# Optimization experiments

Hardware: AMD Instinct MI355X
Metric: run time of the kernel (lower is better)

## Reference

```python
import jax, jax.numpy as jnp
import numpy as np

PI = 3.1415927410125732
N = 4096
L = 1.28e-3          # box side [m]
VEL = 5e-7
RC = 3.15e-6         # Rc = diameter/2
RR = 8e-6
RO = 2.5e-5
RA = np.inf
DT_TRANS = 1.4e-14   # DT (translational diffusion)
DR = 0.0028
GAMMA = 25.0
DT = 0.2             # timestep dt
COLL_ITERS = 30      # fixed cap for collision-resolution do-while (orig caps at 1000)


def setup_inputs() -> dict:
    key = jax.random.key(0)
    ks = jax.random.split(key, 7)
    pos_re = jax.random.uniform(ks[0], (N,), jnp.float32) * L
    pos_im = jax.random.uniform(ks[1], (N,), jnp.float32) * L
    ang = jax.random.uniform(ks[2], (N,), jnp.float32, -PI, PI)
    ori_re = jnp.cos(ang)
    ori_im = jnp.sin(ang)
    deltas = jax.random.uniform(ks[3], (N,), jnp.float32) * 0.5
    rot_noise = jax.random.normal(ks[4], (N,), jnp.float32)
    tn_re = jax.random.normal(ks[5], (N,), jnp.float32)
    tn_im = jax.random.normal(ks[6], (N,), jnp.float32)
    return {"pos_re": pos_re, "pos_im": pos_im, "ori_re": ori_re, "ori_im": ori_im,
            "deltas": deltas, "rot_noise": rot_noise, "tn_re": tn_re, "tn_im": tn_im}


def _wrap(diff):
    # torch get_anglediff wrap: (-2pi,2pi) -> ~(-pi,pi)
    diff = jnp.where(diff <= -PI, jnp.mod(diff, PI), diff)
    return diff - (diff >= PI).astype(diff.dtype) * (2.0 * PI)


def _anglediff(a, b):
    return _wrap(jnp.angle(a) - jnp.angle(b))


def _cossim(a, b):
    # nn.CosineSimilarity(dim=1, eps=1e-14) on view_as_real vectors
    dot = a.real * b.real + a.imag * b.imag
    na = jnp.maximum(jnp.abs(a), 1e-14)
    nb = jnp.maximum(jnp.abs(b), 1e-14)
    return dot / (na * nb)


def _mvc(W, z):
    # real [n,n] mask @ complex [n] vector
    return W @ z.real + 1j * (W @ z.imag)


def _solve_collisions(pos):
    n = pos.shape[0]
    eye_f = jnp.eye(n, dtype=jnp.float32)
    eye_c = eye_f.astype(pos.dtype)

    def step(p):
        diff = p[None, :] - p[:, None] + eye_c  # [i,j] = pos_j - pos_i; diag dummy 1 (nan-safe)
        absd = jnp.abs(diff)
        coll = absd <= (2.0 * RC - eye_f)       # diag threshold negative -> self excluded
        move = jnp.where(coll, diff / jnp.where(coll, absd, 1.0) * ((2.1 * RC - absd) * 0.5), 0.0)
        return p - move.sum(axis=1), coll.sum()

    def body(carry, _):
        p, cont = carry
        p_new, ncoll = step(p)
        p = jnp.where(cont, p_new, p)           # do-while: apply move, then continue if collisions
        return (p, jnp.logical_and(cont, ncoll > 0)), None

    body = jax.checkpoint(body)
    (pos, _), _ = jax.lax.scan(body, (pos, jnp.array(True)), None, length=COLL_ITERS)
    return pos


def _forward(pos_re, pos_im, ori_re, ori_im, deltas, rot_noise, tn_re, tn_im):
    pos = (pos_re + 1j * pos_im).astype(jnp.complex64)
    ori = (ori_re + 1j * ori_im).astype(jnp.complex64)
    n = pos.shape[0]
    eye_b = jnp.eye(n, dtype=bool)

    # pairwise |pos_i - pos_j|; diag made 1 to keep abs() grad-safe (diag is masked out / re-added below)
    dists = jnp.abs(pos[:, None] - pos[None, :] + jnp.eye(n, dtype=pos.dtype))
    mask_rr = (dists <= RR) & ~eye_b              # repulsion zone, self excluded (eye subtracted in orig)
    mask_ro = (dists <= RO + RC) | eye_b          # orientation zone, self included (diag dist 0 in orig)
    mask_ra = (dists <= RA + RC) | eye_b          # Ra = inf -> all ones

    # alpha == 2*pi exactly -> within_view branch skipped (matches original)
    ang = jnp.angle(ori)
    abs_ad = jnp.abs(_wrap(ang[:, None] - ang[None, :]))
    in_front = abs_ad < PI / 2

    Wrr = (mask_rr & in_front).astype(jnp.float32)
    Wro = mask_ro.astype(jnp.float32)
    Wra = mask_ra.astype(jnp.float32)

    n_r = Wrr.sum(axis=1)
    S = _mvc(Wrr, pos) / jnp.maximum(n_r, 1.0) - pos * jnp.sign(n_r)
    d = -S

    n_a = Wra.sum(axis=1)
    cms = _mvc(Wra, pos) / jnp.maximum(n_a, 1.0)
    Ps = cms - pos * jnp.sign(n_a)

    osum = _mvc(Wro, ori)
    left = Ps * jnp.exp(1j * deltas)
    right = Ps * jnp.exp(-1j * deltas)

    # T (=300) >= T_release (=200): choose best turn by cosine similarity
    best = jnp.where(_cossim(left, osum) >= _cossim(right, osum), left, right)

    has_rep = jnp.abs(d) > 0.0
    d_safe = jnp.where(has_rep, d, jnp.ones_like(d))
    att = jnp.where(has_rep, _anglediff(d_safe, ori), _anglediff(best, ori))

    s2dr = np.float32(np.sqrt(2.0 * DR))
    sdt = np.float32(np.sqrt(DT))
    rot = jnp.exp(1j * (DT * GAMMA * DR * jnp.sin(att) + rot_noise * s2dr * sdt))

    # complex standard normal: real/imag each N(0, 1/sqrt(2))
    tnoise = (tn_re + 1j * tn_im) * np.float32(np.sqrt(0.5)) * np.float32(np.sqrt(2.0 * DT_TRANS))
    trans = DT * VEL * ori + tnoise * sdt

    new_pos = _solve_collisions(pos + trans)
    new_ori = ori * rot

    c2r = lambda z: jnp.stack([z.real, z.imag], axis=-1)
    # [5, N, 2]: positions, orientations, orientation_sums, leftturns, rightturns (real views)
    return jnp.stack([c2r(new_pos), c2r(new_ori), c2r(osum), c2r(left), c2r(right)], axis=0)


def reference(pos_re, pos_im, ori_re, ori_im, deltas, rot_noise, tn_re, tn_im):
    return _forward(pos_re, pos_im, ori_re, ori_im, deltas, rot_noise, tn_re, tn_im)
```

## Files before the change

### kernel.cpp

```cpp
#include <hip/hip_runtime.h>

#define NPART 4096
#define PI_F 3.1415927410125732f
#define TWO_PI_F 6.2831854820251465f
#define SENT 4096
#define TILE_F 1.6e-4f
#define HALO_F 2.15e-4f
#define CAP 1280
#define LSENT CAP

__device__ __forceinline__ float wrapf(float d) {
    if (d <= -PI_F) {
        d = fmodf(d, PI_F);
        if (d < 0.0f) d += PI_F;
    }
    if (d >= PI_F) d -= TWO_PI_F;
    return d;
}

__global__ __launch_bounds__(512)
void k_interact(const float* __restrict__ pr, const float* __restrict__ pim,
                const float* __restrict__ orr, const float* __restrict__ oim,
                const float* __restrict__ deltas,
                const float* __restrict__ rot_noise,
                const float* __restrict__ tn_re, const float* __restrict__ tn_im,
                float* __restrict__ out,
                uint2* __restrict__ recQuad, int* __restrict__ recC,
                unsigned short* __restrict__ recNbr16) {
    constexpr float RR_F  = 8e-6f;
    constexpr float RR2   = RR_F * RR_F;
    constexpr float ROC_F = (float)(2.5e-5 + 3.15e-6);
    constexpr float ROC2  = ROC_F * ROC_F;
    constexpr float CUT_F = 14.3e-6f;
    constexpr float CUT2  = CUT_F * CUT_F;

    __shared__ float2 lsP[NPART];
    __shared__ float2 lsO[NPART];
    __shared__ float part[12][64];
    __shared__ float red[12][8];
    __shared__ int ncnt[16];
    __shared__ unsigned short nbrL[16 * 16];

    int tid = threadIdx.x;
    int li = tid & 7, sl = tid >> 3;
    int i0 = blockIdx.x * 16 + li;
    int i1 = i0 + 8;

    if (tid < 16) ncnt[tid] = 0;

    float pxA = pr[i0], pyA = pim[i0], oxA = orr[i0], oyA = oim[i0];
    float pxB = pr[i1], pyB = pim[i1], oxB = orr[i1], oyB = oim[i1];

    float nAr = 0.0f, SAre = 0.0f, SAim = 0.0f, oAre = 0.0f, oAim = 0.0f;
    float nBr = 0.0f, SBre = 0.0f, SBim = 0.0f, oBre = 0.0f, oBim = 0.0f;
    float cs_re = 0.0f, cs_im = 0.0f;

#pragma unroll
    for (int k = 0; k < 8; ++k) {
        int j = k * 512 + tid;
        float jr = pr[j], ji = pim[j];
        lsP[j] = make_float2(jr, ji);
        lsO[j] = make_float2(orr[j], oim[j]);
        cs_re += jr; cs_im += ji;
    }
    __syncthreads();

    for (int c = 0; c < 8; ++c) {
#pragma unroll
        for (int t = 0; t < 8; ++t) {
            int jj = c * 512 + sl * 8 + ((t + sl) & 7);
            int j = jj;
            float2 pv = lsP[jj];
            float drA = pxA - pv.x, diA = pyA - pv.y;
            float d2A = drA * drA + diA * diA;
            float drB = pxB - pv.x, diB = pyB - pv.y;
            float d2B = drB * drB + diB * diB;
            if (__any((d2A <= ROC2) | (d2B <= ROC2))) {
                float2 ov = lsO[jj];
                if (d2A <= ROC2) { oAre += ov.x; oAim += ov.y; }
                float dotA = oxA * ov.x + oyA * ov.y;
                if ((d2A <= RR2) & (dotA > 0.0f) & (j != i0)) {
                    nAr += 1.0f; SAre += pv.x; SAim += pv.y;
                }
                if (d2A <= CUT2 && j != i0) {
                    int slot = atomicAdd(&ncnt[li], 1);
                    if (slot < 16) nbrL[li * 16 + slot] = (unsigned short)j;
                }
                if (d2B <= ROC2) { oBre += ov.x; oBim += ov.y; }
                float dotB = oxB * ov.x + oyB * ov.y;
                if ((d2B <= RR2) & (dotB > 0.0f) & (j != i1)) {
                    nBr += 1.0f; SBre += pv.x; SBim += pv.y;
                }
                if (d2B <= CUT2 && j != i1) {
                    int slot = atomicAdd(&ncnt[li + 8], 1);
                    if (slot < 16) nbrL[(li + 8) * 16 + slot] = (unsigned short)j;
                }
            }
        }
    }

    {
        float v0 = nAr, v1 = SAre, v2 = SAim, v3 = oAre, v4 = oAim;
        float v5 = nBr, v6 = SBre, v7 = SBim, v8 = oBre, v9 = oBim;
        float v10 = cs_re, v11 = cs_im;
#define RED3(v) { v += __shfl_xor(v, 8); v += __shfl_xor(v, 16); v += __shfl_xor(v, 32); }
        RED3(v0) RED3(v1) RED3(v2) RED3(v3) RED3(v4) RED3(v5)
        RED3(v6) RED3(v7) RED3(v8) RED3(v9) RED3(v10) RED3(v11)
#undef RED3
        int lane = tid & 63, wv = tid >> 6;
        if (lane < 8) {
            int col = wv * 8 + lane;
            part[0][col] = v0;  part[1][col] = v1;  part[2][col] = v2;
            part[3][col] = v3;  part[4][col] = v4;  part[5][col] = v5;
            part[6][col] = v6;  part[7][col] = v7;  part[8][col] = v8;
            part[9][col] = v9;  part[10][col] = v10; part[11][col] = v11;
        }
    }
    __syncthreads();
    if (tid < 8) {
#pragma unroll
        for (int av = 0; av < 12; ++av) {
            float s = 0.0f;
#pragma unroll
            for (int w = 0; w < 8; ++w) s += part[av][w * 8 + tid];
            red[av][tid] = s;
        }
    }
    __syncthreads();

    if (tid < 16) {
        int i = blockIdx.x * 16 + tid;
        float n_r, S_re, S_im, o_re, o_im, px, py, ox, oy;
        if (tid < 8) {
            n_r = red[0][tid]; S_re = red[1][tid]; S_im = red[2][tid];
            o_re = red[3][tid]; o_im = red[4][tid];
            px = pxA; py = pyA; ox = oxA; oy = oyA;
        } else {
            int g = tid - 8;
            n_r = red[5][g]; S_re = red[6][g]; S_im = red[7][g];
            o_re = red[8][g]; o_im = red[9][g];
            px = pxB; py = pyB; ox = oxB; oy = oyB;
        }

        float csr_ = 0.0f, csi_ = 0.0f;
#pragma unroll
        for (int k = 0; k < 8; ++k) { csr_ += red[10][k]; csi_ += red[11][k]; }

        float maxnr = fmaxf(n_r, 1.0f);
        float sgn = (n_r > 0.0f) ? 1.0f : 0.0f;
        float Sre = S_re / maxnr - px * sgn;
        float Sim = S_im / maxnr - py * sgn;
        float d_re = -Sre, d_im = -Sim;

        float cmsx = csr_ * (1.0f / 4096.0f);
        float cmsy = csi_ * (1.0f / 4096.0f);
        float Ps_re = cmsx - px;
        float Ps_im = cmsy - py;

        float dl = deltas[i];
        float cd = cosf(dl), sd = sinf(dl);
        float l_re = Ps_re * cd - Ps_im * sd;
        float l_im = Ps_re * sd + Ps_im * cd;
        float r_re = Ps_re * cd + Ps_im * sd;
        float r_im = Ps_im * cd - Ps_re * sd;

        float nb   = fmaxf(hypotf(o_re, o_im), 1e-14f);
        float na_l = fmaxf(hypotf(l_re, l_im), 1e-14f);
        float na_r = fmaxf(hypotf(r_re, r_im), 1e-14f);
        float csl = (l_re * o_re + l_im * o_im) / (na_l * nb);
        float csr2 = (r_re * o_re + r_im * o_im) / (na_r * nb);
        float b_re = (csl >= csr2) ? l_re : r_re;
        float b_im = (csl >= csr2) ? l_im : r_im;

        float ai = atan2f(oy, ox);
        bool has_rep = (d_re != 0.0f) || (d_im != 0.0f);
        float att;
        if (has_rep) att = wrapf(atan2f(d_im, d_re) - ai);
        else         att = wrapf(atan2f(b_im, b_re) - ai);

        constexpr float GDD  = (float)(0.2 * 25.0 * 0.0028);
        constexpr float S2DR = 0.07483314773547883f;
        constexpr float SDT  = 0.44721359549995793f;
        float theta = GDD * sinf(att) + (rot_noise[i] * S2DR) * SDT;
        float rr_ = cosf(theta), ri_ = sinf(theta);

        float no_re = ox * rr_ - oy * ri_;
        float no_im = ox * ri_ + oy * rr_;

        constexpr float DTVEL = (float)(0.2 * 5e-7);
        constexpr float C1 = 0.70710678118654752f;
        constexpr float C2 = 1.6733200530681511e-07f;
        float t_re = DTVEL * ox + ((tn_re[i] * C1) * C2) * SDT;
        float t_im = DTVEL * oy + ((tn_im[i] * C1) * C2) * SDT;
        float p0x = px + t_re, p0y = py + t_im;

        float2* o2 = (float2*)out;
        o2[i]            = make_float2(p0x, p0y);
        o2[1 * 4096 + i] = make_float2(no_re, no_im);
        o2[2 * 4096 + i] = make_float2(o_re, o_im);
        o2[3 * 4096 + i] = make_float2(l_re, l_im);
        o2[4 * 4096 + i] = make_float2(r_re, r_im);

        int c = min(ncnt[tid], 16);
        unsigned q0 = (c > 0) ? nbrL[tid * 16 + 0] : (unsigned)SENT;
        unsigned q1 = (c > 1) ? nbrL[tid * 16 + 1] : (unsigned)SENT;
        unsigned q2 = (c > 2) ? nbrL[tid * 16 + 2] : (unsigned)SENT;
        unsigned q3 = (c > 3) ? nbrL[tid * 16 + 3] : (unsigned)SENT;
        recQuad[i] = make_uint2(q0 | (q1 << 16), q2 | (q3 << 16));
        recC[i] = c;
        if (c > 4) {
            int cp = (c + 3) & ~3;
            for (int m = 4; m < cp; ++m)
                recNbr16[i * 16 + m] = (m < c) ? nbrL[tid * 16 + m]
                                               : (unsigned short)SENT;
        }
    }
}

__global__ __launch_bounds__(256)
void k_coll_tiled(const uint2* __restrict__ recQuad, const int* __restrict__ recC,
                  const unsigned short* __restrict__ recNbr16,
                  float* __restrict__ out) {
    constexpr float TWO_RC  = (float)(2.0 * 3.15e-6);
    constexpr float TWO_RC2 = TWO_RC * TWO_RC;
    constexpr float C21RC   = (float)(2.1 * 3.15e-6);

    __shared__ float2 lpos[CAP + 1];
    __shared__ unsigned short g2l[NPART];
    __shared__ unsigned short lgid[CAP];
    __shared__ uint2 lquad[CAP];
    __shared__ unsigned char lc[CAP];
    __shared__ unsigned char lown[CAP];
    __shared__ short lpool[CAP];
    __shared__ unsigned short pool[96 * 16];
    __shared__ int cnt, poolCnt, flg[2];

    int tid = threadIdx.x;
    int tx = blockIdx.x & 7, ty = blockIdx.x >> 3;
    float x0 = tx * TILE_F, y0 = ty * TILE_F;
    float xlo = (tx == 0) ? -1e9f : x0 - HALO_F;
    float xhi = (tx == 7) ?  1e9f : x0 + TILE_F + HALO_F;
    float ylo = (ty == 0) ? -1e9f : y0 - HALO_F;
    float yhi = (ty == 7) ?  1e9f : y0 + TILE_F + HALO_F;

    if (tid == 0) {
        cnt = 0; poolCnt = 0; flg[0] = 0; flg[1] = 0;
        lpos[LSENT] = make_float2(1e9f, 1e9f);
    }
    __syncthreads();

    const float2* o2in = (const float2*)out;
    for (int g = tid; g < NPART; g += 256) {
        float2 p = o2in[g];
        unsigned short l = 0xFFFF;
        if (p.x >= xlo && p.x < xhi && p.y >= ylo && p.y < yhi) {
            int s = atomicAdd(&cnt, 1);
            if (s < CAP) {
                l = (unsigned short)s;
                lpos[s] = p;
                lgid[s] = (unsigned short)g;
                int ox = min(7, max(0, (int)floorf(p.x * (1.0f / TILE_F))));
                int oy = min(7, max(0, (int)floorf(p.y * (1.0f / TILE_F))));
                lown[s] = (ox == tx && oy == ty) ? 1 : 0;
            }
        }
        g2l[g] = l;
    }
    __syncthreads();
    int n = min(cnt, CAP);

    for (int l = tid; l < n; l += 256) {
        int g = lgid[l];
        uint2 q = recQuad[g];
        int c = recC[g];
        unsigned short a[4] = { (unsigned short)(q.x & 0xffff), (unsigned short)(q.x >> 16),
                                (unsigned short)(q.y & 0xffff), (unsigned short)(q.y >> 16) };
        unsigned short b[4];
#pragma unroll
        for (int k = 0; k < 4; ++k) {
            unsigned short t = (a[k] >= NPART) ? (unsigned short)0xFFFF : g2l[a[k]];
            b[k] = (t == 0xFFFF) ? (unsigned short)LSENT : t;
        }
        lquad[l] = make_uint2((unsigned)b[0] | ((unsigned)b[1] << 16),
                              (unsigned)b[2] | ((unsigned)b[3] << 16));
        lc[l] = (unsigned char)c;
        short prow = -1;
        if (c > 4) {
            int r = atomicAdd(&poolCnt, 1);
            if (r < 96) {
                prow = (short)r;
                int cp = (c + 3) & ~3;
                for (int m = 4; m < cp; ++m) {
                    unsigned short aa = recNbr16[g * 16 + m];
                    unsigned short t = (aa >= NPART) ? (unsigned short)0xFFFF : g2l[aa];
                    pool[r * 16 + m] = (t == 0xFFFF) ? (unsigned short)LSENT : t;
                }
            }
        }
        lpool[l] = prow;
    }
    __syncthreads();

    float nx[5], ny[5];
    int ncs[5];
    for (int it = 0; it < 12; ++it) {
#pragma unroll
        for (int s = 0; s < 5; ++s) {
            ncs[s] = 0;
            int l = s * 256 + tid;
            if (l < n) {
                int c = lc[l];
                if (c > 0) {
                    float2 me = lpos[l];
                    float px = me.x, py = me.y;
                    float mre = 0.0f, mim = 0.0f;
                    int nc = 0;
                    uint2 q = lquad[l];
                    float2 q0 = lpos[q.x & 0xffff], q1 = lpos[q.x >> 16];
                    float2 q2 = lpos[q.y & 0xffff], q3 = lpos[q.y >> 16];
#define COLL_ONE(qq)                                                    \
                    {                                                   \
                        float dr = (qq).x - px, di = (qq).y - py;       \
                        float d2 = dr * dr + di * di;                   \
                        if (d2 <= TWO_RC2) {                            \
                            float a = sqrtf(d2);                        \
                            float mm = (C21RC - a) * 0.5f / a;          \
                            mre += dr * mm; mim += di * mm; ++nc;       \
                        }                                               \
                    }
                    COLL_ONE(q0) COLL_ONE(q1) COLL_ONE(q2) COLL_ONE(q3)
                    for (int m0 = 4; m0 < c; m0 += 4) {
                        int j0, j1, j2, j3;
                        if (lpool[l] >= 0) {
                            const unsigned short* t = &pool[lpool[l] * 16 + m0];
                            j0 = t[0]; j1 = t[1]; j2 = t[2]; j3 = t[3];
                        } else {
                            const unsigned short* t = &recNbr16[(int)lgid[l] * 16 + m0];
                            unsigned short u0 = t[0], u1 = t[1], u2 = t[2], u3 = t[3];
                            j0 = (u0 >= NPART) ? LSENT : (g2l[u0] == 0xFFFF ? LSENT : g2l[u0]);
                            j1 = (u1 >= NPART) ? LSENT : (g2l[u1] == 0xFFFF ? LSENT : g2l[u1]);
                            j2 = (u2 >= NPART) ? LSENT : (g2l[u2] == 0xFFFF ? LSENT : g2l[u2]);
                            j3 = (u3 >= NPART) ? LSENT : (g2l[u3] == 0xFFFF ? LSENT : g2l[u3]);
                        }
                        float2 t0 = lpos[j0], t1 = lpos[j1], t2 = lpos[j2], t3 = lpos[j3];
                        COLL_ONE(t0) COLL_ONE(t1) COLL_ONE(t2) COLL_ONE(t3)
                    }
#undef COLL_ONE
                    ncs[s] = nc;
                    nx[s] = px - mre; ny[s] = py - mim;
                }
            }
        }
        __syncthreads();
        int any = 0;
#pragma unroll
        for (int s = 0; s < 5; ++s) {
            if (ncs[s] > 0) {
                lpos[s * 256 + tid] = make_float2(nx[s], ny[s]);
            }
            any |= ncs[s];
        }
        if (any) flg[it & 1] = 1;
        if (tid == 0) flg[(it + 1) & 1] = 0;
        __syncthreads();
        if (flg[it & 1] == 0) break;
    }

    float2* o2 = (float2*)out;
    for (int l = tid; l < n; l += 256)
        if (lown[l]) o2[lgid[l]] = lpos[l];
}

extern "C" void kernel_launch(void* const* d_in, const int* in_sizes, int n_in,
                              void* d_out, int out_size, void* d_ws, size_t ws_size,
                              hipStream_t stream) {
    const float* pos_re = (const float*)d_in[0];
    const float* pos_im = (const float*)d_in[1];
    const float* ori_re = (const float*)d_in[2];
    const float* ori_im = (const float*)d_in[3];
    const float* deltas = (const float*)d_in[4];
    const float* rot_noise = (const float*)d_in[5];
    const float* tn_re = (const float*)d_in[6];
    const float* tn_im = (const float*)d_in[7];
    float* out = (float*)d_out;

    uint2* recQuad = (uint2*)d_ws;
    int* recC = (int*)(recQuad + NPART);
    unsigned short* recNbr16 = (unsigned short*)(recC + NPART);

    k_interact<<<256, 512, 0, stream>>>(pos_re, pos_im, ori_re, ori_im,
                                        deltas, rot_noise, tn_re, tn_im,
                                        out, recQuad, recC, recNbr16);
    k_coll_tiled<<<64, 256, 0, stream>>>(recQuad, recC, recNbr16, out);
}
```

Measured before the change: 120.8 us.

## Replace block-wide collision solver with single-wavefront-per-tile kernel

Shrinks collision tiles from an 8x8 to a 16x16 grid and runs each tile in one 64-lane wavefront. __syncthreads and shared atomics are replaced by ballot/popcount compaction, compiler memory fences and __any-based convergence checks. The aim is to remove block barrier cost and spread the work over 256 blocks instead of 64. The halo stays 2.15e-4 while the tile shrinks, so each block processes a much larger share of halo particles. The per-thread slot count rises to 14, which adds register pressure, and the smaller CAP and pool limits raise overflow risk.

Measured after the change: 210.2 us. 1.74x slower.

```diff
diff --git a/kernel.cpp b/kernel.cpp
--- a/kernel.cpp
+++ b/kernel.cpp
@@ -4,10 +4,11 @@
 #define PI_F 3.1415927410125732f
 #define TWO_PI_F 6.2831854820251465f
 #define SENT 4096
-#define TILE_F 1.6e-4f
+#define TILE_F 8e-5f
 #define HALO_F 2.15e-4f
-#define CAP 1280
+#define CAP 896
 #define LSENT CAP
+#define SLOTS 14
 
 __device__ __forceinline__ float wrapf(float d) {
     if (d <= -PI_F) {
@@ -217,10 +218,10 @@
     }
 }
 
-__global__ __launch_bounds__(256)
-void k_coll_tiled(const uint2* __restrict__ recQuad, const int* __restrict__ recC,
-                  const unsigned short* __restrict__ recNbr16,
-                  float* __restrict__ out) {
+__global__ __launch_bounds__(64)
+void k_coll_wave(const uint2* __restrict__ recQuad, const int* __restrict__ recC,
+                 const unsigned short* __restrict__ recNbr16,
+                 float* __restrict__ out) {
     constexpr float TWO_RC  = (float)(2.0 * 3.15e-6);
     constexpr float TWO_RC2 = TWO_RC * TWO_RC;
     constexpr float C21RC   = (float)(2.1 * 3.15e-6);
@@ -232,44 +233,47 @@
     __shared__ unsigned char lc[CAP];
     __shared__ unsigned char lown[CAP];
     __shared__ short lpool[CAP];
-    __shared__ unsigned short pool[96 * 16];
-    __shared__ int cnt, poolCnt, flg[2];
-
-    int tid = threadIdx.x;
-    int tx = blockIdx.x & 7, ty = blockIdx.x >> 3;
+    __shared__ unsigned short pool[64 * 16];
+    __shared__ int poolCnt;
+
+    int lane = threadIdx.x;
+    int tx = blockIdx.x & 15, ty = blockIdx.x >> 4;
     float x0 = tx * TILE_F, y0 = ty * TILE_F;
-    float xlo = (tx == 0) ? -1e9f : x0 - HALO_F;
-    float xhi = (tx == 7) ?  1e9f : x0 + TILE_F + HALO_F;
-    float ylo = (ty == 0) ? -1e9f : y0 - HALO_F;
-    float yhi = (ty == 7) ?  1e9f : y0 + TILE_F + HALO_F;
-
-    if (tid == 0) {
-        cnt = 0; poolCnt = 0; flg[0] = 0; flg[1] = 0;
+    float xlo = (tx == 0)  ? -1e9f : x0 - HALO_F;
+    float xhi = (tx == 15) ?  1e9f : x0 + TILE_F + HALO_F;
+    float ylo = (ty == 0)  ? -1e9f : y0 - HALO_F;
+    float yhi = (ty == 15) ?  1e9f : y0 + TILE_F + HALO_F;
+
+    if (lane == 0) {
+        poolCnt = 0;
         lpos[LSENT] = make_float2(1e9f, 1e9f);
     }
-    __syncthreads();
 
     const float2* o2in = (const float2*)out;
-    for (int g = tid; g < NPART; g += 256) {
+    int base = 0;
+    for (int g0 = 0; g0 < NPART; g0 += 64) {
+        int g = g0 + lane;
         float2 p = o2in[g];
+        bool inb = (p.x >= xlo) & (p.x < xhi) & (p.y >= ylo) & (p.y < yhi);
+        unsigned long long m = __ballot(inb);
+        int rank = __popcll(m & ((1ull << lane) - 1ull));
+        int s = base + rank;
         unsigned short l = 0xFFFF;
-        if (p.x >= xlo && p.x < xhi && p.y >= ylo && p.y < yhi) {
-            int s = atomicAdd(&cnt, 1);
-            if (s < CAP) {
-                l = (unsigned short)s;
-                lpos[s] = p;
-                lgid[s] = (unsigned short)g;
-                int ox = min(7, max(0, (int)floorf(p.x * (1.0f / TILE_F))));
-                int oy = min(7, max(0, (int)floorf(p.y * (1.0f / TILE_F))));
-                lown[s] = (ox == tx && oy == ty) ? 1 : 0;
-            }
+        if (inb && s < CAP) {
+            l = (unsigned short)s;
+            lpos[s] = p;
+            lgid[s] = (unsigned short)g;
+            int ox = min(15, max(0, (int)floorf(p.x * (1.0f / TILE_F))));
+            int oy = min(15, max(0, (int)floorf(p.y * (1.0f / TILE_F))));
+            lown[s] = (ox == tx && oy == ty) ? 1 : 0;
         }
         g2l[g] = l;
-    }
-    __syncthreads();
-    int n = min(cnt, CAP);
-
-    for (int l = tid; l < n; l += 256) {
+        base += __popcll(m);
+    }
+    int n = min(base, CAP);
+    asm volatile("" ::: "memory");
+
+    for (int l = lane; l < n; l += 64) {
         int g = lgid[l];
         uint2 q = recQuad[g];
         int c = recC[g];
@@ -287,7 +291,7 @@
         short prow = -1;
         if (c > 4) {
             int r = atomicAdd(&poolCnt, 1);
-            if (r < 96) {
+            if (r < 64) {
                 prow = (short)r;
                 int cp = (c + 3) & ~3;
                 for (int m = 4; m < cp; ++m) {
@@ -299,15 +303,16 @@
         }
         lpool[l] = prow;
     }
-    __syncthreads();
-
-    float nx[5], ny[5];
-    int ncs[5];
+    asm volatile("" ::: "memory");
+
+    float nx[SLOTS], ny[SLOTS];
+    int ncs[SLOTS];
     for (int it = 0; it < 12; ++it) {
-#pragma unroll
-        for (int s = 0; s < 5; ++s) {
+        bool moved = false;
+#pragma unroll
+        for (int s = 0; s < SLOTS; ++s) {
             ncs[s] = 0;
-            int l = s * 256 + tid;
+            int l = s * 64 + lane;
             if (l < n) {
                 int c = lc[l];
                 if (c > 0) {
@@ -351,23 +356,21 @@
                 }
             }
         }
-        __syncthreads();
-        int any = 0;
-#pragma unroll
-        for (int s = 0; s < 5; ++s) {
+        asm volatile("" ::: "memory");
+#pragma unroll
+        for (int s = 0; s < SLOTS; ++s) {
+            int l = s * 64 + lane;
             if (ncs[s] > 0) {
-                lpos[s * 256 + tid] = make_float2(nx[s], ny[s]);
+                lpos[l] = make_float2(nx[s], ny[s]);
+                moved = true;
             }
-            any |= ncs[s];
-        }
-        if (any) flg[it & 1] = 1;
-        if (tid == 0) flg[(it + 1) & 1] = 0;
-        __syncthreads();
-        if (flg[it & 1] == 0) break;
+        }
+        asm volatile("" ::: "memory");
+        if (!__any(moved)) break;
     }
 
     float2* o2 = (float2*)out;
-    for (int l = tid; l < n; l += 256)
+    for (int l = lane; l < n; l += 64)
         if (lown[l]) o2[lgid[l]] = lpos[l];
 }
 
@@ -391,5 +394,5 @@
     k_interact<<<256, 512, 0, stream>>>(pos_re, pos_im, ori_re, ori_im,
                                         deltas, rot_noise, tn_re, tn_im,
                                         out, recQuad, recC, recNbr16);
-    k_coll_tiled<<<64, 256, 0, stream>>>(recQuad, recC, recNbr16, out);
+    k_coll_wave<<<256, 64, 0, stream>>>(recQuad, recC, recNbr16, out);
 }
```
